# Optimization experiments

Hardware: AMD Instinct MI355X
Metric: run time of the kernel (lower is better)

Reference implementation:

```python
import jax, jax.numpy as jnp
import numpy as np

N_NODES = 100000
N_EDGES = 1600000
IN_F, HID_F, OUT_F = 128, 128, 64
BN_EPS = 1e-5


def _glorot(key, shape):
    lim = np.sqrt(6.0 / (shape[0] + shape[1]))
    return jax.random.uniform(key, shape, jnp.float32, -lim, lim)


def setup_inputs() -> dict:
    key = jax.random.key(0)
    ks = jax.random.split(key, 12)
    x = jax.random.normal(ks[0], (N_NODES, IN_F), jnp.float32)
    src = jax.random.randint(ks[1], (N_EDGES,), 0, N_NODES, jnp.int64)
    dst = jax.random.randint(ks[2], (N_EDGES,), 0, N_NODES, jnp.int64)
    dims = [(IN_F, HID_F), (HID_F, HID_F), (HID_F, OUT_F)]
    inp = {"x": x, "src": src, "dst": dst}
    for i, (di, do) in enumerate(dims):
        inp[f"w_self{i}"] = _glorot(ks[3 + 2 * i], (di, do))
        inp[f"w_neigh{i}"] = _glorot(ks[4 + 2 * i], (di, do))
        inp[f"b{i}"] = jnp.zeros((do,), jnp.float32)
    for i in range(2):  # BatchNorm1d(hid) after first two convs
        inp[f"gamma{i}"] = jnp.ones((HID_F,), jnp.float32)
        inp[f"beta{i}"] = jnp.zeros((HID_F,), jnp.float32)
    return inp


def _sage_conv(h, src, dst, w_self, w_neigh, b):
    # mean aggregation over incoming edges: gather src feats, segment-sum by dst
    deg = jax.ops.segment_sum(jnp.ones((src.shape[0],), h.dtype), dst, num_segments=N_NODES)
    agg = jax.ops.segment_sum(h[src], dst, num_segments=N_NODES)
    agg = agg / jnp.maximum(deg, 1.0)[:, None]
    return h @ w_self + agg @ w_neigh + b


def _batchnorm(h, gamma, beta):
    mu = jnp.mean(h, axis=0)
    var = jnp.var(h, axis=0)
    return (h - mu) * jax.lax.rsqrt(var + BN_EPS) * gamma + beta


def reference(x, src, dst, w_self0, w_neigh0, b0, gamma0, beta0,
              w_self1, w_neigh1, b1, gamma1, beta1, w_self2, w_neigh2, b2):
    h = _sage_conv(x, src, dst, w_self0, w_neigh0, b0)
    h = jax.nn.relu(_batchnorm(h, gamma0, beta0))
    h = _sage_conv(h, src, dst, w_self1, w_neigh1, b1)
    h = jax.nn.relu(_batchnorm(h, gamma1, beta1))
    h = _sage_conv(h, src, dst, w_self2, w_neigh2, b2)
    return jax.nn.log_softmax(h, axis=-1)
```

## Files before the change

kernel.cpp:

```cpp
#include <hip/hip_runtime.h>
#include <hip/hip_bf16.h>

typedef unsigned short u16;
typedef unsigned char  u8;
typedef unsigned int   u32;
typedef __attribute__((ext_vector_type(8))) short short8;
typedef __attribute__((ext_vector_type(4))) float floatx4;
typedef __attribute__((ext_vector_type(2))) float floatx2;

__device__ __forceinline__ float bits2f(u32 v){ float f; __builtin_memcpy(&f, &v, 4); return f; }
__device__ __forceinline__ u16 f2bf(float f){
    __hip_bfloat16 h = __float2bfloat16(f);
    u16 u; __builtin_memcpy(&u, &h, 2); return u;
}

__device__ __forceinline__ void gload_lds16(const void* g, void* l){
    __builtin_amdgcn_global_load_lds(
        (const __attribute__((address_space(1))) unsigned char*)g,
        (__attribute__((address_space(3))) unsigned char*)l, 16, 0, 0);
}


__global__ __launch_bounds__(256) void cvt_kernel(const float* __restrict__ in,
                                                  u16* __restrict__ out,
                                                  u32* __restrict__ out8, int total4){
    int i = blockIdx.x * 256 + threadIdx.x;
    if (i >= total4) return;
    float4 v = ((const float4*)in)[i];
    uint2 o;
    o.x = (u32)f2bf(v.x) | ((u32)f2bf(v.y) << 16);
    o.y = (u32)f2bf(v.z) | ((u32)f2bf(v.w) << 16);
    ((uint2*)out)[i] = o;
    u32 p8 = (u32)__builtin_amdgcn_cvt_pk_fp8_f32(v.x, v.y, 0, false);
    p8     = (u32)__builtin_amdgcn_cvt_pk_fp8_f32(v.z, v.w, (int)p8, true);
    out8[i] = p8;
}


__global__ __launch_bounds__(256) void cvt8a_kernel(const u16* __restrict__ in,
                                                    const float* __restrict__ cs,
                                                    uint2* __restrict__ out8, int total8){
    int i = blockIdx.x * 256 + threadIdx.x;
    if (i >= total8) return;
    const int c0 = (i & 15) * 8;
    uint4 v = ((const uint4*)in)[i];
    u32 w[4] = {v.x, v.y, v.z, v.w};
    float f[8];
    #pragma unroll
    for (int j = 0; j < 4; ++j){
        f[2*j]   = bits2f(w[j] << 16);
        f[2*j+1] = bits2f(w[j] & 0xffff0000u);
    }
    #pragma unroll
    for (int j = 0; j < 8; ++j)
        f[j] = fmaxf(fmaf(f[j], cs[256 + c0 + j], cs[384 + c0 + j]), 0.f);
    u32 lo = (u32)__builtin_amdgcn_cvt_pk_fp8_f32(f[0], f[1], 0, false);
    lo     = (u32)__builtin_amdgcn_cvt_pk_fp8_f32(f[2], f[3], (int)lo, true);
    u32 hi = (u32)__builtin_amdgcn_cvt_pk_fp8_f32(f[4], f[5], 0, false);
    hi     = (u32)__builtin_amdgcn_cvt_pk_fp8_f32(f[6], f[7], (int)hi, true);
    uint2 o; o.x = lo; o.y = hi;
    out8[i] = o;
}


__global__ __launch_bounds__(256) void bhist_kernel(const int* __restrict__ dst,
                                                    int* __restrict__ gbcnt, int E){
    __shared__ int bc[256];
    const int t = threadIdx.x;
    bc[t] = 0;
    __syncthreads();
    const int tile0 = blockIdx.x * 8192;
    const int cnt = min(8192, E - tile0);
    for (int j = t; j < cnt; j += 256) atomicAdd(&bc[dst[tile0 + j] >> 9], 1);
    __syncthreads();
    if (bc[t] > 0) atomicAdd(&gbcnt[t], bc[t]);
}

__global__ __launch_bounds__(256) void bscan_kernel(const int* __restrict__ gbcnt,
                                                    int* __restrict__ bbase,
                                                    int* __restrict__ bcur, int nbuk){
    __shared__ int ws[4];
    const int t = threadIdx.x, lane = t & 63, wv = t >> 6;
    int v = (t < nbuk) ? gbcnt[t] : 0;
    int s = v;
    for (int off = 1; off < 64; off <<= 1){
        int n = __shfl_up(s, off);
        if (lane >= off) s += n;
    }
    if (lane == 63) ws[wv] = s;
    __syncthreads();
    int woff = 0;
    for (int w = 0; w < wv; ++w) woff += ws[w];
    int excl = s + woff - v;
    if (t < nbuk){ bbase[t] = excl; bcur[t] = excl; }
}

#define BIN_TILE 8192
__global__ __launch_bounds__(256) void bin_kernel(const int* __restrict__ src,
                                                  const int* __restrict__ dst,
                                                  int* __restrict__ bcur,
                                                  u32* __restrict__ pairs, int E, int nbuk){
    __shared__ u32 hcnt[256], hexcl[256], hoff[256];
    __shared__ int gbase[256];
    __shared__ u32 stage[BIN_TILE];
    __shared__ unsigned char bkt[BIN_TILE];
    const int t = threadIdx.x;
    const int tile0 = blockIdx.x * BIN_TILE;
    const int cntE = min(BIN_TILE, E - tile0);

    hcnt[t] = 0;
    __syncthreads();
    for (int j = t; j < cntE; j += 256){
        int d = dst[tile0 + j];
        atomicAdd(&hcnt[d >> 9], 1u);
    }
    __syncthreads();
    if (t < 64){
        u32 a0 = hcnt[4*t], a1 = hcnt[4*t+1], a2 = hcnt[4*t+2], a3 = hcnt[4*t+3];
        u32 lsum = a0 + a1 + a2 + a3;
        u32 s = lsum;
        for (int off = 1; off < 64; off <<= 1){
            u32 n = __shfl_up(s, off);
            if (t >= off) s += n;
        }
        u32 base = s - lsum;
        hexcl[4*t]   = base;
        hexcl[4*t+1] = base + a0;
        hexcl[4*t+2] = base + a0 + a1;
        hexcl[4*t+3] = base + a0 + a1 + a2;
        hoff[4*t]   = base;
        hoff[4*t+1] = base + a0;
        hoff[4*t+2] = base + a0 + a1;
        hoff[4*t+3] = base + a0 + a1 + a2;
    }
    __syncthreads();
    if (t < nbuk && hcnt[t] > 0) gbase[t] = atomicAdd(&bcur[t], (int)hcnt[t]);
    for (int j = t; j < cntE; j += 256){
        int d = dst[tile0 + j];
        int s = src[tile0 + j];
        int b = d >> 9;
        u32 p = atomicAdd(&hoff[b], 1u);
        stage[p] = ((u32)s << 9) | (u32)(d & 511);
        bkt[p] = (unsigned char)b;
    }
    __syncthreads();
    for (int j = t; j < cntE; j += 256){
        int b = bkt[j];
        pairs[gbase[b] + (int)((u32)j - hexcl[b])] = stage[j];
    }
}

__global__ __launch_bounds__(256) void sort2_kernel(const u32* __restrict__ pairs,
                                                    const int* __restrict__ bbase,
                                                    int* __restrict__ indptr,
                                                    float* __restrict__ invdeg,
                                                    int* __restrict__ esrc,
                                                    int M, int E, int nbuk){
    __shared__ int ndeg[512];
    __shared__ int cur[512];
    __shared__ int wsI[4];
    const int b = blockIdx.x;
    const int node0 = b * 512;
    const int lo = bbase[b];
    const int hi = (b + 1 < nbuk) ? bbase[b + 1] : E;
    const int t = threadIdx.x, lane = t & 63, wv = t >> 6;

    ndeg[t] = 0; ndeg[t + 256] = 0;
    __syncthreads();
    for (int i = lo + t; i < hi; i += 256) atomicAdd(&ndeg[pairs[i] & 511], 1);
    __syncthreads();

    const int d0 = ndeg[2*t], d1 = ndeg[2*t + 1];
    const int p = d0 + d1;
    int s = p;
    for (int off = 1; off < 64; off <<= 1){
        int n = __shfl_up(s, off);
        if (lane >= off) s += n;
    }
    if (lane == 63) wsI[wv] = s;
    __syncthreads();
    int woff = 0;
    for (int w = 0; w < wv; ++w) woff += wsI[w];
    const int incl = s + woff;
    const int excl0 = incl - p;
    const int excl1 = excl0 + d0;

    const int n0 = node0 + 2*t, n1 = node0 + 2*t + 1;
    if (n0 < M){
        indptr[n0 + 1] = lo + excl0 + d0;
        invdeg[n0] = 1.0f / (float)max(d0, 1);
        cur[2*t] = lo + excl0;
    }
    if (n1 < M){
        indptr[n1 + 1] = lo + excl1 + d1;
        invdeg[n1] = 1.0f / (float)max(d1, 1);
        cur[2*t + 1] = lo + excl1;
    }
    if (b == 0 && t == 0) indptr[0] = 0;
    __syncthreads();
    for (int i = lo + t; i < hi; i += 256){
        u32 v = pairs[i];
        int pos = atomicAdd(&cur[v & 511], 1);
        esrc[pos] = (int)(v >> 9);
    }
}


__global__ __launch_bounds__(256) void pack3_kernel(const float* __restrict__ w0s, const float* __restrict__ w0n,
                                                    const float* __restrict__ w1s, const float* __restrict__ w1n,
                                                    const float* __restrict__ w2s, const float* __restrict__ w2n,
                                                    u16* __restrict__ bp0, u16* __restrict__ bp1,
                                                    u16* __restrict__ bp2){
    int i = blockIdx.x * 256 + threadIdx.x;
    const float *ws, *wn; u16* bp; int N;
    if (i < 32768){ ws = w0s; wn = w0n; bp = bp0; N = 128; }
    else if (i < 65536){ i -= 32768; ws = w1s; wn = w1n; bp = bp1; N = 128; }
    else { i -= 65536; ws = w2s; wn = w2n; bp = bp2; N = 64; }
    int n = i >> 8, k = i & 255;
    float v = (k < 128) ? ws[k * N + n] : wn[(k - 128) * N + n];
    bp[i] = f2bf(v);
}


__global__ __launch_bounds__(256) void agg_kernel(const u8* __restrict__ h8,
                                                  const int* __restrict__ indptr,
                                                  const int* __restrict__ esrc,
                                                  const float* __restrict__ invdeg,
                                                  u16* __restrict__ agg, int M){
    const int l8 = threadIdx.x & 7;
    const int n = (blockIdx.x * 256 + threadIdx.x) >> 3;
    if (n >= M) return;
    const int beg = indptr[n];
    const int end = indptr[n + 1];
    const float fs = invdeg[n];

    floatx2 acc[8];
    #pragma unroll
    for (int i = 0; i < 8; ++i){ acc[i].x = 0.f; acc[i].y = 0.f; }

    const u8* hb = h8 + l8 * 16;

    auto accum = [&](uint4 v){
        u32 w[4] = {v.x, v.y, v.z, v.w};
        #pragma unroll
        for (int j = 0; j < 4; ++j){
            acc[2*j]   += __builtin_amdgcn_cvt_pk_f32_fp8(w[j], false);
            acc[2*j+1] += __builtin_amdgcn_cvt_pk_f32_fp8(w[j], true);
        }
    };

    int e = beg;
    for (; e + 4 <= end; e += 4){
        const int i0 = esrc[e];
        const int i1 = esrc[e + 1];
        const int i2 = esrc[e + 2];
        const int i3 = esrc[e + 3];
        uint4 v0 = *(const uint4*)(hb + (size_t)i0 * 128);
        uint4 v1 = *(const uint4*)(hb + (size_t)i1 * 128);
        uint4 v2 = *(const uint4*)(hb + (size_t)i2 * 128);
        uint4 v3 = *(const uint4*)(hb + (size_t)i3 * 128);
        accum(v0); accum(v1); accum(v2); accum(v3);
    }
    for (; e < end; ++e){
        const int i0 = esrc[e];
        uint4 v0 = *(const uint4*)(hb + (size_t)i0 * 128);
        accum(v0);
    }

    u32 o[8];
    #pragma unroll
    for (int k = 0; k < 8; ++k)
        o[k] = (u32)f2bf(acc[k].x * fs) | ((u32)f2bf(acc[k].y * fs) << 16);
    uint4 w0 = {o[0], o[1], o[2], o[3]};
    uint4 w1 = {o[4], o[5], o[6], o[7]};
    *(uint4*)(agg + (size_t)n * 128 + l8 * 16)     = w0;
    *(uint4*)(agg + (size_t)n * 128 + l8 * 16 + 8) = w1;
}


template<int NTW, bool STATS, bool AFFA, bool LSM>
__global__ __launch_bounds__(256, 4) void gemm3_kernel(const u16* __restrict__ hA,
                                                       const u16* __restrict__ aggA,
                                                       const u16* __restrict__ Bp,
                                                       const float* __restrict__ bias,
                                                       const float* __restrict__ cs,
                                                       void* __restrict__ outPre,
                                                       float* __restrict__ partials,
                                                       int M, int T, int GBs){
    constexpr int N = NTW * 64;
    __shared__ __align__(16) u16 Abuf[3][4096];
    __shared__ __align__(16) char cbuf[2][4352];
    __shared__ float s_sc[128], s_sh[128];

    const int wave = threadIdx.x >> 6;
    const int lane = threadIdx.x & 63;
    const int m15 = lane & 15;
    const int quad = lane >> 4;
    const int colbase = wave * (NTW * 16);

    if (AFFA && threadIdx.x < 128){
        s_sc[threadIdx.x] = cs[256 + threadIdx.x];
        s_sh[threadIdx.x] = cs[384 + threadIdx.x];
    }
    __syncthreads();

    short8 breg[NTW][8];
    float bv[NTW];
    #pragma unroll
    for (int nt = 0; nt < NTW; ++nt){
        bv[nt] = bias[colbase + nt * 16 + m15];
        #pragma unroll
        for (int k0 = 0; k0 < 8; ++k0)
            breg[nt][k0] = *(const short8*)(Bp + (size_t)(colbase + nt * 16 + m15) * 256 + k0 * 32 + quad * 8);
    }

    float sS[NTW], sQ[NTW];
    #pragma unroll
    for (int nt = 0; nt < NTW; ++nt){ sS[nt] = 0.f; sQ[nt] = 0.f; }

    auto stage = [&](int bufIdx, int tile){
        const int srow = lane & 15, squad = lane >> 4;
        int arow = tile * 16 + srow;
        if (arow >= M) arow = M - 1;
        #pragma unroll
        for (int h = 0; h < 2; ++h){
            const int k0 = wave * 2 + h;
            const u16* base = (k0 < 4) ? hA : aggA;
            const u16* g = base + (size_t)arow * 128 + (k0 & 3) * 32 + squad * 8;
            gload_lds16(g, &Abuf[bufIdx][k0 * 512]);
        }
    };

    const int t0 = blockIdx.x;
    const int nIter = (T - 1 - t0) / GBs + 1;

    stage(0, t0);
    if (nIter > 1) stage(1, t0 + GBs);

    int t = t0;
    for (int it = 0; it < nIter; ++it){
        const int cur = it % 3;
        if (it + 2 < nIter) stage((it + 2) % 3, t + 2 * GBs);

        const int ahead = min(nIter - 1 - it, 2);
        if (ahead >= 2)      asm volatile("s_waitcnt vmcnt(4)" ::: "memory");
        else if (ahead == 1) asm volatile("s_waitcnt vmcnt(2)" ::: "memory");
        else                 asm volatile("s_waitcnt vmcnt(0)" ::: "memory");
        __builtin_amdgcn_s_barrier();
        __builtin_amdgcn_sched_barrier(0);

        floatx4 acc[NTW];
        #pragma unroll
        for (int nt = 0; nt < NTW; ++nt) acc[nt] = 0.0f;
        #pragma unroll
        for (int k0 = 0; k0 < 8; ++k0){
            short8 a = *(const short8*)&Abuf[cur][k0 * 512 + quad * 128 + m15 * 8];
            if (AFFA && k0 < 4){
                const int cb = k0 * 32 + quad * 8;
                #pragma unroll
                for (int j = 0; j < 8; ++j){
                    float f = bits2f(((u32)(u16)a[j]) << 16);
                    f = fmaxf(fmaf(f, s_sc[cb + j], s_sh[cb + j]), 0.f);
                    a[j] = (short)f2bf(f);
                }
            }
            #pragma unroll
            for (int nt = 0; nt < NTW; ++nt)
                acc[nt] = __builtin_amdgcn_mfma_f32_16x16x32_bf16(a, breg[nt][k0], acc[nt], 0, 0, 0);
        }

        char* cb = &cbuf[it & 1][0];
        const int r0 = quad * 4;
        #pragma unroll
        for (int nt = 0; nt < NTW; ++nt){
            const int col = colbase + nt * 16 + m15;
            #pragma unroll
            for (int r = 0; r < 4; ++r){
                float v = acc[nt][r] + bv[nt];
                if (STATS){
                    int row = t * 16 + r0 + r;
                    if (row < M){
                        sS[nt] += v;
                        sQ[nt] = fmaf(v, v, sQ[nt]);
                    }
                    ((u16*)cb)[(r0 + r) * 136 + col] = f2bf(v);
                } else {
                    ((float*)cb)[(r0 + r) * 68 + col] = v;
                }
            }
        }
        asm volatile("s_waitcnt lgkmcnt(0)" ::: "memory");
        __builtin_amdgcn_s_barrier();
        __builtin_amdgcn_sched_barrier(0);

        const int srow = threadIdx.x >> 4, seg = threadIdx.x & 15;
        const int grow = t * 16 + srow;
        if (LSM){
            float4 w = *(const float4*)((const float*)cb + srow * 68 + seg * 4);
            float m = fmaxf(fmaxf(w.x, w.y), fmaxf(w.z, w.w));
            m = fmaxf(m, __shfl_xor(m, 1));
            m = fmaxf(m, __shfl_xor(m, 2));
            m = fmaxf(m, __shfl_xor(m, 4));
            m = fmaxf(m, __shfl_xor(m, 8));
            float e = __expf(w.x - m) + __expf(w.y - m) + __expf(w.z - m) + __expf(w.w - m);
            e += __shfl_xor(e, 1);
            e += __shfl_xor(e, 2);
            e += __shfl_xor(e, 4);
            e += __shfl_xor(e, 8);
            float lg = m + __logf(e);
            if (grow < M){
                float4 o;
                o.x = w.x - lg; o.y = w.y - lg; o.z = w.z - lg; o.w = w.w - lg;
                *(float4*)((float*)outPre + (size_t)grow * 64 + seg * 4) = o;
            }
        } else if (grow < M){
            if (STATS){
                uint4 w = *(const uint4*)((const u16*)cb + srow * 136 + seg * 8);
                *(uint4*)((u16*)outPre + (size_t)grow * N + seg * 8) = w;
            } else {
                float4 w = *(const float4*)((const float*)cb + srow * 68 + seg * 4);
                *(float4*)((float*)outPre + (size_t)grow * N + seg * 4) = w;
            }
        }
        t += GBs;
    }

    if (STATS){
        #pragma unroll
        for (int nt = 0; nt < NTW; ++nt){
            float s = sS[nt], q = sQ[nt];
            s += __shfl_xor(s, 16);  s += __shfl_xor(s, 32);
            q += __shfl_xor(q, 16);  q += __shfl_xor(q, 32);
            if (quad == 0){
                const int c = colbase + nt * 16 + m15;
                partials[(size_t)c * GBs + blockIdx.x]         = s;
                partials[(size_t)(128 + c) * GBs + blockIdx.x] = q;
            }
        }
    }
}


__global__ __launch_bounds__(256) void bnstat_kernel(const float* __restrict__ partials,
                                                     float* __restrict__ cs,
                                                     const float* __restrict__ gamma,
                                                     const float* __restrict__ beta,
                                                     float invM, int GB){
    const int wv = threadIdx.x >> 6, lane = threadIdx.x & 63;
    const int c = blockIdx.x * 4 + wv;
    float s = 0.f, q = 0.f;
    const float* ps = partials + (size_t)c * GB;
    const float* pq = partials + (size_t)(128 + c) * GB;
    for (int k = lane; k < GB; k += 64){ s += ps[k]; q += pq[k]; }
    #pragma unroll
    for (int o = 32; o; o >>= 1){ s += __shfl_xor(s, o); q += __shfl_xor(q, o); }
    if (lane == 0){
        float mu  = s * invM;
        float var = fmaxf(q * invM - mu * mu, 0.f);
        float sc  = gamma[c] * rsqrtf(var + 1e-5f);
        cs[256 + c] = sc;
        cs[384 + c] = beta[c] - mu * sc;
    }
}


extern "C" void kernel_launch(void* const* d_in, const int* in_sizes, int n_in,
                              void* d_out, int out_size, void* d_ws, size_t ws_size,
                              hipStream_t stream) {
    const float* x   = (const float*)d_in[0];
    const int*   src = (const int*)d_in[1];
    const int*   dst = (const int*)d_in[2];
    const float* wself[3]  = {(const float*)d_in[3], (const float*)d_in[6], (const float*)d_in[9]};
    const float* wneigh[3] = {(const float*)d_in[4], (const float*)d_in[7], (const float*)d_in[10]};
    const float* bias[3]   = {(const float*)d_in[5], (const float*)d_in[8], (const float*)d_in[11]};
    const float* gamma[2]  = {(const float*)d_in[12], (const float*)d_in[14]};
    const float* beta[2]   = {(const float*)d_in[13], (const float*)d_in[15]};

    const int M = in_sizes[0] / 128;
    const int E = in_sizes[1];
    const int NBUK = (M + 511) / 512;
    const int T = (M + 15) / 16;
    const int GB = 1024;

    char* ws = (char*)d_ws;
    size_t off = 0;
    auto alloc = [&](size_t bytes) -> void* {
        void* p = ws + off;
        off = (off + bytes + 511) & ~(size_t)511;
        return p;
    };
    int*   gbcnt  = (int*)alloc(256 * 4);
    int*   bbase  = (int*)alloc(256 * 4);
    int*   bcur   = (int*)alloc(256 * 4);
    int*   indptr = (int*)alloc((size_t)(M + 1) * 4);
    u32*   pairs  = (u32*)alloc((size_t)E * 4);
    int*   esrc   = (int*)alloc((size_t)E * 4);
    float* invdeg = (float*)alloc((size_t)M * 4);
    u16* bpack0 = (u16*)alloc(128 * 256 * 2);
    u16* bpack1 = (u16*)alloc(128 * 256 * 2);
    u16* bpack2 = (u16*)alloc(64 * 256 * 2);
    float* colstat0 = (float*)alloc(512 * 4);
    float* colstat1 = (float*)alloc(512 * 4);
    float* partials = (float*)alloc((size_t)GB * 256 * 4);
    u16*   hbuf   = (u16*)alloc((size_t)M * 128 * 2);
    u16*   aggbuf = (u16*)alloc((size_t)M * 128 * 2);
    u16*   preA   = (u16*)alloc((size_t)M * 128 * 2);
    u16*   preB   = (u16*)alloc((size_t)M * 128 * 2);
    u8*    x8     = (u8*)alloc((size_t)M * 128);
    u8*    preA8  = (u8*)alloc((size_t)M * 128);
    u8*    preB8  = (u8*)alloc((size_t)M * 128);

    hipMemsetAsync(gbcnt, 0, 256 * 4, stream);
    bhist_kernel<<<(E + 8191) / 8192, 256, 0, stream>>>(dst, gbcnt, E);
    bscan_kernel<<<1, 256, 0, stream>>>(gbcnt, bbase, bcur, NBUK);
    bin_kernel<<<(E + BIN_TILE - 1) / BIN_TILE, 256, 0, stream>>>(src, dst, bcur, pairs, E, NBUK);
    sort2_kernel<<<NBUK, 256, 0, stream>>>(pairs, bbase, indptr, invdeg, esrc, M, E, NBUK);

    cvt_kernel<<<((M * 32) + 255) / 256, 256, 0, stream>>>(x, hbuf, (u32*)x8, M * 32);
    pack3_kernel<<<320, 256, 0, stream>>>(wself[0], wneigh[0], wself[1], wneigh[1],
                                          wself[2], wneigh[2], bpack0, bpack1, bpack2);

    agg_kernel<<<(M + 31) / 32, 256, 0, stream>>>(x8, indptr, esrc, invdeg, aggbuf, M);
    gemm3_kernel<2, true, false, false><<<GB, 256, 0, stream>>>(hbuf, aggbuf, bpack0, bias[0], nullptr,
                                                                preA, partials, M, T, GB);
    bnstat_kernel<<<32, 256, 0, stream>>>(partials, colstat0, gamma[0], beta[0], 1.0f / (float)M, GB);
    cvt8a_kernel<<<((M * 16) + 255) / 256, 256, 0, stream>>>(preA, colstat0, (uint2*)preA8, M * 16);

    agg_kernel<<<(M + 31) / 32, 256, 0, stream>>>(preA8, indptr, esrc, invdeg, aggbuf, M);
    gemm3_kernel<2, true, true, false><<<GB, 256, 0, stream>>>(preA, aggbuf, bpack1, bias[1], colstat0,
                                                               preB, partials, M, T, GB);
    bnstat_kernel<<<32, 256, 0, stream>>>(partials, colstat1, gamma[1], beta[1], 1.0f / (float)M, GB);
    cvt8a_kernel<<<((M * 16) + 255) / 256, 256, 0, stream>>>(preB, colstat1, (uint2*)preB8, M * 16);

    agg_kernel<<<(M + 31) / 32, 256, 0, stream>>>(preB8, indptr, esrc, invdeg, aggbuf, M);
    gemm3_kernel<1, false, true, true><<<GB, 256, 0, stream>>>(preB, aggbuf, bpack2, bias[2], colstat1,
                                                               d_out, partials, M, T, GB);
}
```

Before: 402.0 us.

## Merge prep kernels, fold BN stats into atomics, deepen agg gather unroll

Combines the fp32-to-bf16/fp8 conversion, destination histogram and weight packing into one launch. The bnstat reduction kernel is removed: the GEMM epilogue now atomically adds per-column sums into zeroed colstat buffers, and consumers derive scale and shift on the fly. The aggregation loop is unrolled to 8 edges to keep more gathers in flight. Together these cut launch count and partials traffic, at the cost of global float atomic contention and non-deterministic summation order.

```diff
diff --git a/kernel.cpp b/kernel.cpp
--- a/kernel.cpp
+++ b/kernel.cpp
@@ -21,25 +21,67 @@
 }
 
 
-__global__ __launch_bounds__(256) void cvt_kernel(const float* __restrict__ in,
-                                                  u16* __restrict__ out,
-                                                  u32* __restrict__ out8, int total4){
-    int i = blockIdx.x * 256 + threadIdx.x;
-    if (i >= total4) return;
-    float4 v = ((const float4*)in)[i];
-    uint2 o;
-    o.x = (u32)f2bf(v.x) | ((u32)f2bf(v.y) << 16);
-    o.y = (u32)f2bf(v.z) | ((u32)f2bf(v.w) << 16);
-    ((uint2*)out)[i] = o;
-    u32 p8 = (u32)__builtin_amdgcn_cvt_pk_fp8_f32(v.x, v.y, 0, false);
-    p8     = (u32)__builtin_amdgcn_cvt_pk_fp8_f32(v.z, v.w, (int)p8, true);
-    out8[i] = p8;
+__global__ __launch_bounds__(256) void prep_kernel(const float* __restrict__ x,
+                                                   u16* __restrict__ hbuf,
+                                                   u32* __restrict__ x8, int total4, int nCvtB,
+                                                   const int* __restrict__ dst,
+                                                   int* __restrict__ gbcnt, int E, int nHistB,
+                                                   const float* __restrict__ w0s, const float* __restrict__ w0n,
+                                                   const float* __restrict__ w1s, const float* __restrict__ w1n,
+                                                   const float* __restrict__ w2s, const float* __restrict__ w2n,
+                                                   u16* __restrict__ bp0, u16* __restrict__ bp1,
+                                                   u16* __restrict__ bp2){
+    const int b = blockIdx.x;
+    if (b < nCvtB){
+        int i = b * 256 + threadIdx.x;
+        if (i >= total4) return;
+        float4 v = ((const float4*)x)[i];
+        uint2 o;
+        o.x = (u32)f2bf(v.x) | ((u32)f2bf(v.y) << 16);
+        o.y = (u32)f2bf(v.z) | ((u32)f2bf(v.w) << 16);
+        ((uint2*)hbuf)[i] = o;
+        u32 p8 = (u32)__builtin_amdgcn_cvt_pk_fp8_f32(v.x, v.y, 0, false);
+        p8     = (u32)__builtin_amdgcn_cvt_pk_fp8_f32(v.z, v.w, (int)p8, true);
+        x8[i] = p8;
+    } else if (b < nCvtB + nHistB){
+        __shared__ int bc[256];
+        const int t = threadIdx.x;
+        bc[t] = 0;
+        __syncthreads();
+        const int tile0 = (b - nCvtB) * 8192;
+        const int cnt = min(8192, E - tile0);
+        for (int j = t; j < cnt; j += 256) atomicAdd(&bc[dst[tile0 + j] >> 9], 1);
+        __syncthreads();
+        if (bc[t] > 0) atomicAdd(&gbcnt[t], bc[t]);
+    } else {
+        int i = (b - nCvtB - nHistB) * 256 + threadIdx.x;
+        const float *ws, *wn; u16* bp; int N;
+        if (i < 32768){ ws = w0s; wn = w0n; bp = bp0; N = 128; }
+        else if (i < 65536){ i -= 32768; ws = w1s; wn = w1n; bp = bp1; N = 128; }
+        else { i -= 65536; ws = w2s; wn = w2n; bp = bp2; N = 64; }
+        int n = i >> 8, k = i & 255;
+        float v = (k < 128) ? ws[k * N + n] : wn[(k - 128) * N + n];
+        bp[i] = f2bf(v);
+    }
 }
 
 
 __global__ __launch_bounds__(256) void cvt8a_kernel(const u16* __restrict__ in,
                                                     const float* __restrict__ cs,
+                                                    const float* __restrict__ gamma,
+                                                    const float* __restrict__ beta,
+                                                    float invM,
                                                     uint2* __restrict__ out8, int total8){
+    __shared__ float s_sc[128], s_sh[128];
+    if (threadIdx.x < 128){
+        const int c = threadIdx.x;
+        float mu  = cs[c] * invM;
+        float var = fmaxf(cs[128 + c] * invM - mu * mu, 0.f);
+        float sc  = gamma[c] * rsqrtf(var + 1e-5f);
+        s_sc[c] = sc;
+        s_sh[c] = beta[c] - mu * sc;
+    }
+    __syncthreads();
     int i = blockIdx.x * 256 + threadIdx.x;
     if (i >= total8) return;
     const int c0 = (i & 15) * 8;
@@ -53,7 +95,7 @@
     }
     #pragma unroll
     for (int j = 0; j < 8; ++j)
-        f[j] = fmaxf(fmaf(f[j], cs[256 + c0 + j], cs[384 + c0 + j]), 0.f);
+        f[j] = fmaxf(fmaf(f[j], s_sc[c0 + j], s_sh[c0 + j]), 0.f);
     u32 lo = (u32)__builtin_amdgcn_cvt_pk_fp8_f32(f[0], f[1], 0, false);
     lo     = (u32)__builtin_amdgcn_cvt_pk_fp8_f32(f[2], f[3], (int)lo, true);
     u32 hi = (u32)__builtin_amdgcn_cvt_pk_fp8_f32(f[4], f[5], 0, false);
@@ -62,19 +104,6 @@
     out8[i] = o;
 }
 
-
-__global__ __launch_bounds__(256) void bhist_kernel(const int* __restrict__ dst,
-                                                    int* __restrict__ gbcnt, int E){
-    __shared__ int bc[256];
-    const int t = threadIdx.x;
-    bc[t] = 0;
-    __syncthreads();
-    const int tile0 = blockIdx.x * 8192;
-    const int cnt = min(8192, E - tile0);
-    for (int j = t; j < cnt; j += 256) atomicAdd(&bc[dst[tile0 + j] >> 9], 1);
-    __syncthreads();
-    if (bc[t] > 0) atomicAdd(&gbcnt[t], bc[t]);
-}
 
 __global__ __launch_bounds__(256) void bscan_kernel(const int* __restrict__ gbcnt,
                                                     int* __restrict__ bbase,
@@ -206,22 +235,6 @@
 }
 
 
-__global__ __launch_bounds__(256) void pack3_kernel(const float* __restrict__ w0s, const float* __restrict__ w0n,
-                                                    const float* __restrict__ w1s, const float* __restrict__ w1n,
-                                                    const float* __restrict__ w2s, const float* __restrict__ w2n,
-                                                    u16* __restrict__ bp0, u16* __restrict__ bp1,
-                                                    u16* __restrict__ bp2){
-    int i = blockIdx.x * 256 + threadIdx.x;
-    const float *ws, *wn; u16* bp; int N;
-    if (i < 32768){ ws = w0s; wn = w0n; bp = bp0; N = 128; }
-    else if (i < 65536){ i -= 32768; ws = w1s; wn = w1n; bp = bp1; N = 128; }
-    else { i -= 65536; ws = w2s; wn = w2n; bp = bp2; N = 64; }
-    int n = i >> 8, k = i & 255;
-    float v = (k < 128) ? ws[k * N + n] : wn[(k - 128) * N + n];
-    bp[i] = f2bf(v);
-}
-
-
 __global__ __launch_bounds__(256) void agg_kernel(const u8* __restrict__ h8,
                                                   const int* __restrict__ indptr,
                                                   const int* __restrict__ esrc,
@@ -250,20 +263,29 @@
     };
 
     int e = beg;
-    for (; e + 4 <= end; e += 4){
-        const int i0 = esrc[e];
-        const int i1 = esrc[e + 1];
-        const int i2 = esrc[e + 2];
-        const int i3 = esrc[e + 3];
-        uint4 v0 = *(const uint4*)(hb + (size_t)i0 * 128);
-        uint4 v1 = *(const uint4*)(hb + (size_t)i1 * 128);
-        uint4 v2 = *(const uint4*)(hb + (size_t)i2 * 128);
-        uint4 v3 = *(const uint4*)(hb + (size_t)i3 * 128);
-        accum(v0); accum(v1); accum(v2); accum(v3);
+    for (; e + 8 <= end; e += 8){
+        int idx[8];
+        #pragma unroll
+        for (int u = 0; u < 8; ++u) idx[u] = esrc[e + u];
+        uint4 v[8];
+        #pragma unroll
+        for (int u = 0; u < 8; ++u) v[u] = *(const uint4*)(hb + (size_t)idx[u] * 128);
+        #pragma unroll
+        for (int u = 0; u < 8; ++u) accum(v[u]);
+    }
+    if (e + 4 <= end){
+        int idx[4];
+        #pragma unroll
+        for (int u = 0; u < 4; ++u) idx[u] = esrc[e + u];
+        uint4 v[4];
+        #pragma unroll
+        for (int u = 0; u < 4; ++u) v[u] = *(const uint4*)(hb + (size_t)idx[u] * 128);
+        #pragma unroll
+        for (int u = 0; u < 4; ++u) accum(v[u]);
+        e += 4;
     }
     for (; e < end; ++e){
-        const int i0 = esrc[e];
-        uint4 v0 = *(const uint4*)(hb + (size_t)i0 * 128);
+        uint4 v0 = *(const uint4*)(hb + (size_t)esrc[e] * 128);
         accum(v0);
     }
 
@@ -284,8 +306,11 @@
                                                        const u16* __restrict__ Bp,
                                                        const float* __restrict__ bias,
                                                        const float* __restrict__ cs,
+                                                       const float* __restrict__ gammaA,
+                                                       const float* __restrict__ betaA,
+                                                       float invM,
                                                        void* __restrict__ outPre,
-                                                       float* __restrict__ partials,
+                                                       float* __restrict__ csOut,
                                                        int M, int T, int GBs){
     constexpr int N = NTW * 64;
     __shared__ __align__(16) u16 Abuf[3][4096];
@@ -299,8 +324,12 @@
     const int colbase = wave * (NTW * 16);
 
     if (AFFA && threadIdx.x < 128){
-        s_sc[threadIdx.x] = cs[256 + threadIdx.x];
-        s_sh[threadIdx.x] = cs[384 + threadIdx.x];
+        const int c = threadIdx.x;
+        float mu  = cs[c] * invM;
+        float var = fmaxf(cs[128 + c] * invM - mu * mu, 0.f);
+        float sc  = gammaA[c] * rsqrtf(var + 1e-5f);
+        s_sc[c] = sc;
+        s_sh[c] = betaA[c] - mu * sc;
     }
     __syncthreads();
 
@@ -433,33 +462,10 @@
             q += __shfl_xor(q, 16);  q += __shfl_xor(q, 32);
             if (quad == 0){
                 const int c = colbase + nt * 16 + m15;
-                partials[(size_t)c * GBs + blockIdx.x]         = s;
-                partials[(size_t)(128 + c) * GBs + blockIdx.x] = q;
+                atomicAdd(&csOut[c], s);
+                atomicAdd(&csOut[128 + c], q);
             }
         }
-    }
-}
-
-
-__global__ __launch_bounds__(256) void bnstat_kernel(const float* __restrict__ partials,
-                                                     float* __restrict__ cs,
-                                                     const float* __restrict__ gamma,
-                                                     const float* __restrict__ beta,
-                                                     float invM, int GB){
-    const int wv = threadIdx.x >> 6, lane = threadIdx.x & 63;
-    const int c = blockIdx.x * 4 + wv;
-    float s = 0.f, q = 0.f;
-    const float* ps = partials + (size_t)c * GB;
-    const float* pq = partials + (size_t)(128 + c) * GB;
-    for (int k = lane; k < GB; k += 64){ s += ps[k]; q += pq[k]; }
-    #pragma unroll
-    for (int o = 32; o; o >>= 1){ s += __shfl_xor(s, o); q += __shfl_xor(q, o); }
-    if (lane == 0){
-        float mu  = s * invM;
-        float var = fmaxf(q * invM - mu * mu, 0.f);
-        float sc  = gamma[c] * rsqrtf(var + 1e-5f);
-        cs[256 + c] = sc;
-        cs[384 + c] = beta[c] - mu * sc;
     }
 }
 
@@ -481,6 +487,7 @@
     const int NBUK = (M + 511) / 512;
     const int T = (M + 15) / 16;
     const int GB = 1024;
+    const float invM = 1.0f / (float)M;
 
     char* ws = (char*)d_ws;
     size_t off = 0;
@@ -489,7 +496,10 @@
         off = (off + bytes + 511) & ~(size_t)511;
         return p;
     };
-    int*   gbcnt  = (int*)alloc(256 * 4);
+    int*   gbcnt    = (int*)alloc(256 * 4);
+    float* colstat0 = (float*)alloc(512 * 4);
+    float* colstat1 = (float*)alloc(512 * 4);
+    const size_t zbytes = off;
     int*   bbase  = (int*)alloc(256 * 4);
     int*   bcur   = (int*)alloc(256 * 4);
     int*   indptr = (int*)alloc((size_t)(M + 1) * 4);
@@ -499,9 +509,6 @@
     u16* bpack0 = (u16*)alloc(128 * 256 * 2);
     u16* bpack1 = (u16*)alloc(128 * 256 * 2);
     u16* bpack2 = (u16*)alloc(64 * 256 * 2);
-    float* colstat0 = (float*)alloc(512 * 4);
-    float* colstat1 = (float*)alloc(512 * 4);
-    float* partials = (float*)alloc((size_t)GB * 256 * 4);
     u16*   hbuf   = (u16*)alloc((size_t)M * 128 * 2);
     u16*   aggbuf = (u16*)alloc((size_t)M * 128 * 2);
     u16*   preA   = (u16*)alloc((size_t)M * 128 * 2);
@@ -510,29 +517,36 @@
     u8*    preA8  = (u8*)alloc((size_t)M * 128);
     u8*    preB8  = (u8*)alloc((size_t)M * 128);
 
-    hipMemsetAsync(gbcnt, 0, 256 * 4, stream);
-    bhist_kernel<<<(E + 8191) / 8192, 256, 0, stream>>>(dst, gbcnt, E);
+    hipMemsetAsync(ws, 0, zbytes, stream);
+
+    const int nCvtB  = (M * 32 + 255) / 256;
+    const int nHistB = (E + 8191) / 8192;
+    prep_kernel<<<nCvtB + nHistB + 320, 256, 0, stream>>>(
+        x, hbuf, (u32*)x8, M * 32, nCvtB,
+        dst, gbcnt, E, nHistB,
+        wself[0], wneigh[0], wself[1], wneigh[1], wself[2], wneigh[2],
+        bpack0, bpack1, bpack2);
+
     bscan_kernel<<<1, 256, 0, stream>>>(gbcnt, bbase, bcur, NBUK);
     bin_kernel<<<(E + BIN_TILE - 1) / BIN_TILE, 256, 0, stream>>>(src, dst, bcur, pairs, E, NBUK);
     sort2_kernel<<<NBUK, 256, 0, stream>>>(pairs, bbase, indptr, invdeg, esrc, M, E, NBUK);
 
-    cvt_kernel<<<((M * 32) + 255) / 256, 256, 0, stream>>>(x, hbuf, (u32*)x8, M * 32);
-    pack3_kernel<<<320, 256, 0, stream>>>(wself[0], wneigh[0], wself[1], wneigh[1],
-                                          wself[2], wneigh[2], bpack0, bpack1, bpack2);
-
     agg_kernel<<<(M + 31) / 32, 256, 0, stream>>>(x8, indptr, esrc, invdeg, aggbuf, M);
-    gemm3_kernel<2, true, false, false><<<GB, 256, 0, stream>>>(hbuf, aggbuf, bpack0, bias[0], nullptr,
-                                                                preA, partials, M, T, GB);
-    bnstat_kernel<<<32, 256, 0, stream>>>(partials, colstat0, gamma[0], beta[0], 1.0f / (float)M, GB);
-    cvt8a_kernel<<<((M * 16) + 255) / 256, 256, 0, stream>>>(preA, colstat0, (uint2*)preA8, M * 16);
+    gemm3_kernel<2, true, false, false><<<GB, 256, 0, stream>>>(hbuf, aggbuf, bpack0, bias[0],
+                                                                nullptr, nullptr, nullptr, invM,
+                                                                preA, colstat0, M, T, GB);
+    cvt8a_kernel<<<(M * 16 + 255) / 256, 256, 0, stream>>>(preA, colstat0, gamma[0], beta[0], invM,
+                                                           (uint2*)preA8, M * 16);
 
     agg_kernel<<<(M + 31) / 32, 256, 0, stream>>>(preA8, indptr, esrc, invdeg, aggbuf, M);
-    gemm3_kernel<2, true, true, false><<<GB, 256, 0, stream>>>(preA, aggbuf, bpack1, bias[1], colstat0,
-                                                               preB, partials, M, T, GB);
-    bnstat_kernel<<<32, 256, 0, stream>>>(partials, colstat1, gamma[1], beta[1], 1.0f / (float)M, GB);
-    cvt8a_kernel<<<((M * 16) + 255) / 256, 256, 0, stream>>>(preB, colstat1, (uint2*)preB8, M * 16);
+    gemm3_kernel<2, true, true, false><<<GB, 256, 0, stream>>>(preA, aggbuf, bpack1, bias[1],
+                                                               colstat0, gamma[0], beta[0], invM,
+                                                               preB, colstat1, M, T, GB);
+    cvt8a_kernel<<<(M * 16 + 255) / 256, 256, 0, stream>>>(preB, colstat1, gamma[1], beta[1], invM,
+                                                           (uint2*)preB8, M * 16);
 
     agg_kernel<<<(M + 31) / 32, 256, 0, stream>>>(preB8, indptr, esrc, invdeg, aggbuf, M);
-    gemm3_kernel<1, false, true, true><<<GB, 256, 0, stream>>>(preB, aggbuf, bpack2, bias[2], colstat1,
-                                                               d_out, partials, M, T, GB);
-}
+    gemm3_kernel<1, false, true, true><<<GB, 256, 0, stream>>>(preB, aggbuf, bpack2, bias[2],
+                                                               colstat1, gamma[1], beta[1], invM,
+                                                               d_out, nullptr, M, T, GB);
+}
```

Result: slower. 415.2 us (+3.3%).
